# Performance work log

Measured on AMD Instinct MI355X. Metric: run time of the kernel, lower is better.

## Reference

```python
import jax, jax.numpy as jnp
import numpy as np


def _cdist(p1, p2):
    # Euclidean cdist via the matmul expansion (matches torch.cdist p=2 fast path):
    # ||a-b||^2 = ||a||^2 + ||b||^2 - 2 a.b ; clamp tiny negatives before sqrt.
    sq1 = jnp.sum(p1 * p1, axis=-1, keepdims=True)        # (N, 1)
    sq2 = jnp.sum(p2 * p2, axis=-1, keepdims=True).T      # (1, M)
    d2 = sq1 + sq2 - 2.0 * (p1 @ p2.T)                    # (N, M)
    return jnp.sqrt(jnp.maximum(d2, 0.0))


def setup_inputs() -> dict:
    key = jax.random.key(0)
    k1, k2 = jax.random.split(key)
    N, M = 16384, 16384
    points1 = jax.random.normal(k1, (N, 3), dtype=jnp.float32)
    points2 = jax.random.normal(k2, (M, 3), dtype=jnp.float32)
    return {"points1": points1, "points2": points2}


def reference(points1, points2):
    dist = _cdist(points1, points2)                        # (N, M)
    min1 = jnp.min(dist, axis=1)                           # (N,) nearest in points2
    min2 = jnp.min(dist, axis=0)                           # (M,) nearest in points1
    return jnp.sum(min1) + jnp.sum(min2)
```

## Files before the change

kernel.cpp:

```cpp
#include <hip/hip_runtime.h>
#include <hip/hip_bf16.h>
#include <math.h>


typedef _Float16 half8    __attribute__((ext_vector_type(8)));
typedef float    floatx16 __attribute__((ext_vector_type(16)));

constexpr int CH   = 4096;
constexpr int ROWS = 128;
constexpr int BLK  = 256;

__global__ __launch_bounds__(256) void pack_kernel(
    const float* __restrict__ P1, const float* __restrict__ P2,
    uint2* __restrict__ F1, uint2* __restrict__ F2,
    int n1, int n2, int NP, float* __restrict__ out)
{
    int i = blockIdx.x * 256 + threadIdx.x;
    if (i == 0) out[0] = 0.0f;
    const float* P; uint2* F; int n, idx;
    if (i < NP)          { P = P1; F = F1; n = n1; idx = i; }
    else if (i < 2 * NP) { P = P2; F = F2; n = n2; idx = i - NP; }
    else return;
    int j = idx < n ? idx : n - 1;
    float x = P[3*j], y = P[3*j+1], z = P[3*j+2];
    _Float16 hx = (_Float16)x, hy = (_Float16)y, hz = (_Float16)z;
    float qx = (float)hx, qy = (float)hy, qz = (float)hz;
    _Float16 hw = (_Float16)(qx*qx + qy*qy + qz*qz);
    union { _Float16 h[4]; uint2 u; } p;
    p.h[0] = hx; p.h[1] = hy; p.h[2] = hz; p.h[3] = hw;
    F[idx] = p.u;
}

__global__ __launch_bounds__(BLK, 4) void chamfer_sweep_kernel(
    const uint2* __restrict__ F1, const uint2* __restrict__ F2,
    float* __restrict__ part, int n1, int n2, int YC)
{
    __shared__ uint2 sB[CH];
    __shared__ float sRowMin[ROWS];

    const int dir   = blockIdx.z;
    const uint2* FA = dir == 0 ? F1 : F2;
    const uint2* FB = dir == 0 ? F2 : F1;
    const int nA    = dir == 0 ? n1 : n2;
    float* pbase    = part + (dir == 0 ? 0 : (size_t)YC * n1);

    const int tid  = threadIdx.x;
    const int wave = tid >> 6;
    const int lane = tid & 63;
    const int n    = lane & 31;
    const int g    = lane >> 5;
    const bool g0  = (g == 0);

    {
        const uint4* src = (const uint4*)(FB + (size_t)blockIdx.y * CH);
        uint4* dst = (uint4*)sB;
        for (int i = tid; i < CH / 2; i += BLK) dst[i] = src[i];
    }

    const _Float16 h0 = (_Float16)0.0f;
    half8 af;
    {
        int arow = blockIdx.x * ROWS + wave * 32 + n;
        union { uint2 u; _Float16 h[4]; } au; au.u = FA[arow];
        const _Float16 m2 = (_Float16)(-2.0f);
        af[0] = g0 ? (_Float16)(au.h[0] * m2) : h0;
        af[1] = g0 ? (_Float16)(au.h[1] * m2) : h0;
        af[2] = g0 ? (_Float16)(au.h[2] * m2) : h0;
        af[3] = g0 ? (_Float16)1.0f : h0;
        af[4] = g0 ? au.h[3] : h0;
        af[5] = h0; af[6] = h0; af[7] = h0;
    }

    __syncthreads();

    floatx16 rowmin;
#pragma unroll
    for (int r = 0; r < 16; ++r) rowmin[r] = 1e30f;
    const floatx16 zacc = {};

    union BF { half8 v; unsigned u[4]; uint2 lo; };
    BF bu0, bu1, bu2, bu3;
    { union { _Float16 h[2]; unsigned u; } q;
      q.h[0] = (_Float16)1.0f; q.h[1] = h0;
      bu0.u[2] = q.u; bu0.u[3] = 0u;
      bu1.u[2] = q.u; bu1.u[3] = 0u;
      bu2.u[2] = q.u; bu2.u[3] = 0u;
      bu3.u[2] = q.u; bu3.u[3] = 0u; }

    for (int bt = 0; bt < CH / 128; ++bt) {
        const uint2* p = sB + bt * 128 + n;
        bu0.lo = p[0];
        bu1.lo = p[32];
        bu2.lo = p[64];
        bu3.lo = p[96];

        floatx16 d0 = __builtin_amdgcn_mfma_f32_32x32x16_f16(af, bu0.v, zacc, 0, 0, 0);
        floatx16 d1 = __builtin_amdgcn_mfma_f32_32x32x16_f16(af, bu1.v, zacc, 0, 0, 0);
        floatx16 d2 = __builtin_amdgcn_mfma_f32_32x32x16_f16(af, bu2.v, zacc, 0, 0, 0);
        floatx16 d3 = __builtin_amdgcn_mfma_f32_32x32x16_f16(af, bu3.v, zacc, 0, 0, 0);

#pragma unroll
        for (int r = 0; r < 16; ++r) {
            float t = fminf(fminf(rowmin[r], d0[r]), d1[r]);
            rowmin[r] = fminf(fminf(t, d2[r]), d3[r]);
        }
    }

#pragma unroll
    for (int mask = 1; mask <= 16; mask <<= 1)
#pragma unroll
        for (int r = 0; r < 16; ++r)
            rowmin[r] = fminf(rowmin[r], __shfl_xor(rowmin[r], mask));

    if (n == 0) {
#pragma unroll
        for (int r = 0; r < 16; ++r) {
            int rr = wave * 32 + g * 4 + ((r & 3) + 8 * (r >> 2));
            sRowMin[rr] = rowmin[r];
        }
    }
    __syncthreads();

    if (tid < ROWS) {
        int grow = blockIdx.x * ROWS + tid;
        if (grow < nA) pbase[(size_t)grow * YC + blockIdx.y] = sRowMin[tid];
    }
}

__global__ __launch_bounds__(256) void reduce_kernel(
    const float* __restrict__ part, float* __restrict__ out,
    int ntot, int YC)
{
    __shared__ float s[256];
    int r = blockIdx.x * 256 + threadIdx.x;
    float acc = 0.0f;
    if (r < ntot) {
        float m;
        if (YC == 4) {
            const float4 v = ((const float4*)part)[r];
            m = fminf(fminf(v.x, v.y), fminf(v.z, v.w));
        } else {
            const float* p = part + (size_t)r * YC;
            m = 1e30f;
            for (int y = 0; y < YC; ++y) m = fminf(m, p[y]);
        }
        acc = sqrtf(fmaxf(m, 0.0f));
    }
    s[threadIdx.x] = acc;
    __syncthreads();
    for (int w = 128; w > 0; w >>= 1) {
        if (threadIdx.x < w) s[threadIdx.x] += s[threadIdx.x + w];
        __syncthreads();
    }
    if (threadIdx.x == 0) atomicAdd(out, s[0]);
}

extern "C" void kernel_launch(void* const* d_in, const int* in_sizes, int n_in,
                              void* d_out, int out_size, void* d_ws, size_t ws_size,
                              hipStream_t stream) {
    const float* P1 = (const float*)d_in[0];
    const float* P2 = (const float*)d_in[1];
    const int n1 = in_sizes[0] / 3;
    const int n2 = in_sizes[1] / 3;
    const int nmax = (n1 > n2) ? n1 : n2;
    const int YC = (nmax + CH - 1) / CH;
    const int NP = YC * CH;

    uint2* F1   = (uint2*)d_ws;
    uint2* F2   = F1 + NP;
    float* part = (float*)(F2 + NP);
    float* out  = (float*)d_out;

    pack_kernel<<<(2 * NP + 255) / 256, 256, 0, stream>>>(P1, P2, F1, F2, n1, n2, NP, out);

    {
        dim3 grid(NP / ROWS, YC, 2);
        chamfer_sweep_kernel<<<grid, BLK, 0, stream>>>(F1, F2, part, n1, n2, YC);
    }
    reduce_kernel<<<(n1 + n2 + 255) / 256, 256, 0, stream>>>(part, out, n1 + n2, YC);
}
```

Before: 77.18 us.

## Fuse pack, sweep and reduce into one cooperative kernel with grid syncs

Merges the pack, distance-sweep and reduce stages into a single cooperative kernel, separated by grid-wide barriers. It falls back to the original three launches if the cooperative launch fails. The aim is to remove two kernel launches and the idle gaps between them. The price is two grid syncs, and the fused path only runs if all 1024 blocks can be resident at once. The reduce stage now uses 32 threads per block with a warp-shuffle sum.

```diff
diff --git a/kernel.cpp b/kernel.cpp
--- a/kernel.cpp
+++ b/kernel.cpp
@@ -1,6 +1,9 @@
 #include <hip/hip_runtime.h>
+#include <hip/hip_cooperative_groups.h>
 #include <hip/hip_bf16.h>
 #include <math.h>
+
+namespace cg = cooperative_groups;
 
 
 typedef _Float16 half8    __attribute__((ext_vector_type(8)));
@@ -10,28 +13,18 @@
 constexpr int ROWS = 128;
 constexpr int BLK  = 256;
 
-__global__ __launch_bounds__(256) void pack_kernel(
-    const float* __restrict__ P1, const float* __restrict__ P2,
-    uint2* __restrict__ F1, uint2* __restrict__ F2,
-    int n1, int n2, int NP, float* __restrict__ out)
-{
-    int i = blockIdx.x * 256 + threadIdx.x;
-    if (i == 0) out[0] = 0.0f;
-    const float* P; uint2* F; int n, idx;
-    if (i < NP)          { P = P1; F = F1; n = n1; idx = i; }
-    else if (i < 2 * NP) { P = P2; F = F2; n = n2; idx = i - NP; }
-    else return;
-    int j = idx < n ? idx : n - 1;
+__device__ __forceinline__ uint2 pack_point(const float* __restrict__ P, int j)
+{
     float x = P[3*j], y = P[3*j+1], z = P[3*j+2];
     _Float16 hx = (_Float16)x, hy = (_Float16)y, hz = (_Float16)z;
     float qx = (float)hx, qy = (float)hy, qz = (float)hz;
     _Float16 hw = (_Float16)(qx*qx + qy*qy + qz*qz);
     union { _Float16 h[4]; uint2 u; } p;
     p.h[0] = hx; p.h[1] = hy; p.h[2] = hz; p.h[3] = hw;
-    F[idx] = p.u;
-}
-
-__global__ __launch_bounds__(BLK, 4) void chamfer_sweep_kernel(
+    return p.u;
+}
+
+__device__ __forceinline__ void sweep_body(
     const uint2* __restrict__ F1, const uint2* __restrict__ F2,
     float* __restrict__ part, int n1, int n2, int YC)
 {
@@ -125,6 +118,71 @@
         int grow = blockIdx.x * ROWS + tid;
         if (grow < nA) pbase[(size_t)grow * YC + blockIdx.y] = sRowMin[tid];
     }
+}
+
+__global__ __launch_bounds__(BLK, 4) void chamfer_fused_kernel(
+    const float* __restrict__ P1, const float* __restrict__ P2,
+    uint2* __restrict__ F1, uint2* __restrict__ F2,
+    float* __restrict__ part, float* __restrict__ out,
+    int n1, int n2, int YC, int NP)
+{
+    cg::grid_group gg = cg::this_grid();
+    const int fb = blockIdx.x + gridDim.x * (blockIdx.y + gridDim.y * blockIdx.z);
+
+    {
+        int i = fb * BLK + threadIdx.x;
+        if (i == 0) out[0] = 0.0f;
+        if (i < 2 * NP) {
+            if (i < NP) { int j = i < n1 ? i : n1 - 1;            F1[i]      = pack_point(P1, j); }
+            else        { int i2 = i - NP; int j = i2 < n2 ? i2 : n2 - 1; F2[i2] = pack_point(P2, j); }
+        }
+    }
+    gg.sync();
+
+    sweep_body(F1, F2, part, n1, n2, YC);
+    gg.sync();
+
+    {
+        const int ntot = n1 + n2;
+        if (threadIdx.x < 32) {
+            int r = fb * 32 + threadIdx.x;
+            float acc = 0.0f;
+            if (r < ntot) {
+                float m;
+                if (YC == 4) {
+                    const float4 v = ((const float4*)part)[r];
+                    m = fminf(fminf(v.x, v.y), fminf(v.z, v.w));
+                } else {
+                    const float* p = part + (size_t)r * YC;
+                    m = 1e30f;
+                    for (int y = 0; y < YC; ++y) m = fminf(m, p[y]);
+                }
+                acc = sqrtf(fmaxf(m, 0.0f));
+            }
+#pragma unroll
+            for (int mask = 1; mask <= 16; mask <<= 1)
+                acc += __shfl_xor(acc, mask, 32);
+            if (threadIdx.x == 0) atomicAdd(out, acc);
+        }
+    }
+}
+
+__global__ __launch_bounds__(256) void pack_kernel(
+    const float* __restrict__ P1, const float* __restrict__ P2,
+    uint2* __restrict__ F1, uint2* __restrict__ F2,
+    int n1, int n2, int NP, float* __restrict__ out)
+{
+    int i = blockIdx.x * 256 + threadIdx.x;
+    if (i == 0) out[0] = 0.0f;
+    if (i < NP)          { int j = i < n1 ? i : n1 - 1;               F1[i]      = pack_point(P1, j); }
+    else if (i < 2 * NP) { int i2 = i - NP; int j = i2 < n2 ? i2 : n2 - 1; F2[i2] = pack_point(P2, j); }
+}
+
+__global__ __launch_bounds__(BLK, 4) void chamfer_sweep_kernel(
+    const uint2* __restrict__ F1, const uint2* __restrict__ F2,
+    float* __restrict__ part, int n1, int n2, int YC)
+{
+    sweep_body(F1, F2, part, n1, n2, YC);
 }
 
 __global__ __launch_bounds__(256) void reduce_kernel(
@@ -171,11 +229,18 @@
     float* part = (float*)(F2 + NP);
     float* out  = (float*)d_out;
 
-    pack_kernel<<<(2 * NP + 255) / 256, 256, 0, stream>>>(P1, P2, F1, F2, n1, n2, NP, out);
-
-    {
-        dim3 grid(NP / ROWS, YC, 2);
+    dim3 grid(NP / ROWS, YC, 2);
+
+    void* args[] = { (void*)&P1, (void*)&P2, (void*)&F1, (void*)&F2,
+                     (void*)&part, (void*)&out,
+                     (void*)&n1, (void*)&n2, (void*)&YC, (void*)&NP };
+    hipError_t err = hipLaunchCooperativeKernel(
+        (void*)chamfer_fused_kernel, grid, dim3(BLK), args, 0, stream);
+
+    if (err != hipSuccess) {
+        (void)hipGetLastError();
+        pack_kernel<<<(2 * NP + 255) / 256, 256, 0, stream>>>(P1, P2, F1, F2, n1, n2, NP, out);
         chamfer_sweep_kernel<<<grid, BLK, 0, stream>>>(F1, F2, part, n1, n2, YC);
-    }
-    reduce_kernel<<<(n1 + n2 + 255) / 256, 256, 0, stream>>>(part, out, n1 + n2, YC);
-}
+        reduce_kernel<<<(n1 + n2 + 255) / 256, 256, 0, stream>>>(part, out, n1 + n2, YC);
+    }
+}
```

Measured after the change: 308.0 us. 3.99x slower.

## Stage full point set in LDS per block and fuse reduction into sweep kernel

Applied to the files above, without the earlier changes.

Each block now loads the entire opposite point set (up to 16384 points, 128KB) into shared memory instead of a 4096-point chunk. The grid loses its Y dimension, the partial-min buffer goes away, and the sqrt plus sum happen in the sweep kernel with one atomic per block, which removes the separate reduce kernel. The inner loop also software-prefetches the next tile's LDS operands. In exchange, the large LDS footprint limits occupancy to roughly one block per CU, the grid is four times smaller, and inputs larger than 16384 points would be silently truncated.

```diff
diff --git a/kernel.cpp b/kernel.cpp
--- a/kernel.cpp
+++ b/kernel.cpp
@@ -6,9 +6,20 @@
 typedef _Float16 half8    __attribute__((ext_vector_type(8)));
 typedef float    floatx16 __attribute__((ext_vector_type(16)));
 
-constexpr int CH   = 4096;
-constexpr int ROWS = 128;
-constexpr int BLK  = 256;
+constexpr int CHMAX = 16384;
+constexpr int ROWS  = 128;
+constexpr int BLK   = 256;
+
+__device__ __forceinline__ uint2 pack_point(const float* __restrict__ P, int j)
+{
+    float x = P[3*j], y = P[3*j+1], z = P[3*j+2];
+    _Float16 hx = (_Float16)x, hy = (_Float16)y, hz = (_Float16)z;
+    float qx = (float)hx, qy = (float)hy, qz = (float)hz;
+    _Float16 hw = (_Float16)(qx*qx + qy*qy + qz*qz);
+    union { _Float16 h[4]; uint2 u; } p;
+    p.h[0] = hx; p.h[1] = hy; p.h[2] = hz; p.h[3] = hw;
+    return p.u;
+}
 
 __global__ __launch_bounds__(256) void pack_kernel(
     const float* __restrict__ P1, const float* __restrict__ P2,
@@ -17,32 +28,21 @@
 {
     int i = blockIdx.x * 256 + threadIdx.x;
     if (i == 0) out[0] = 0.0f;
-    const float* P; uint2* F; int n, idx;
-    if (i < NP)          { P = P1; F = F1; n = n1; idx = i; }
-    else if (i < 2 * NP) { P = P2; F = F2; n = n2; idx = i - NP; }
-    else return;
-    int j = idx < n ? idx : n - 1;
-    float x = P[3*j], y = P[3*j+1], z = P[3*j+2];
-    _Float16 hx = (_Float16)x, hy = (_Float16)y, hz = (_Float16)z;
-    float qx = (float)hx, qy = (float)hy, qz = (float)hz;
-    _Float16 hw = (_Float16)(qx*qx + qy*qy + qz*qz);
-    union { _Float16 h[4]; uint2 u; } p;
-    p.h[0] = hx; p.h[1] = hy; p.h[2] = hz; p.h[3] = hw;
-    F[idx] = p.u;
+    if (i < NP)          { int j = i < n1 ? i : n1 - 1;                    F1[i]  = pack_point(P1, j); }
+    else if (i < 2 * NP) { int i2 = i - NP; int j = i2 < n2 ? i2 : n2 - 1; F2[i2] = pack_point(P2, j); }
 }
 
-__global__ __launch_bounds__(BLK, 4) void chamfer_sweep_kernel(
+__global__ __launch_bounds__(BLK) void chamfer_sweep_kernel(
     const uint2* __restrict__ F1, const uint2* __restrict__ F2,
-    float* __restrict__ part, int n1, int n2, int YC)
+    float* __restrict__ out, int n1, int n2, int NP)
 {
-    __shared__ uint2 sB[CH];
-    __shared__ float sRowMin[ROWS];
+    __shared__ uint2 sB[CHMAX];
+    __shared__ float sSum[8];
 
     const int dir   = blockIdx.z;
     const uint2* FA = dir == 0 ? F1 : F2;
     const uint2* FB = dir == 0 ? F2 : F1;
     const int nA    = dir == 0 ? n1 : n2;
-    float* pbase    = part + (dir == 0 ? 0 : (size_t)YC * n1);
 
     const int tid  = threadIdx.x;
     const int wave = tid >> 6;
@@ -52,9 +52,9 @@
     const bool g0  = (g == 0);
 
     {
-        const uint4* src = (const uint4*)(FB + (size_t)blockIdx.y * CH);
+        const uint4* src = (const uint4*)FB;
         uint4* dst = (uint4*)sB;
-        for (int i = tid; i < CH / 2; i += BLK) dst[i] = src[i];
+        for (int i = tid; i < NP / 2; i += BLK) dst[i] = src[i];
     }
 
     const _Float16 h0 = (_Float16)0.0f;
@@ -87,12 +87,18 @@
       bu2.u[2] = q.u; bu2.u[3] = 0u;
       bu3.u[2] = q.u; bu3.u[3] = 0u; }
 
-    for (int bt = 0; bt < CH / 128; ++bt) {
-        const uint2* p = sB + bt * 128 + n;
-        bu0.lo = p[0];
-        bu1.lo = p[32];
-        bu2.lo = p[64];
-        bu3.lo = p[96];
+    const int NT = NP / 128;
+    const uint2* p0 = sB + n;
+    uint2 c0 = p0[0], c1 = p0[32], c2 = p0[64], c3 = p0[96];
+
+    for (int bt = 0; bt < NT; ++bt) {
+        const uint2* pn = sB + (bt + 1 < NT ? (bt + 1) * 128 : 0) + n;
+        uint2 f0 = pn[0], f1 = pn[32], f2 = pn[64], f3 = pn[96];
+
+        bu0.lo = c0;
+        bu1.lo = c1;
+        bu2.lo = c2;
+        bu3.lo = c3;
 
         floatx16 d0 = __builtin_amdgcn_mfma_f32_32x32x16_f16(af, bu0.v, zacc, 0, 0, 0);
         floatx16 d1 = __builtin_amdgcn_mfma_f32_32x32x16_f16(af, bu1.v, zacc, 0, 0, 0);
@@ -104,6 +110,8 @@
             float t = fminf(fminf(rowmin[r], d0[r]), d1[r]);
             rowmin[r] = fminf(fminf(t, d2[r]), d3[r]);
         }
+
+        c0 = f0; c1 = f1; c2 = f2; c3 = f3;
     }
 
 #pragma unroll
@@ -112,47 +120,23 @@
         for (int r = 0; r < 16; ++r)
             rowmin[r] = fminf(rowmin[r], __shfl_xor(rowmin[r], mask));
 
+    float acc = 0.0f;
     if (n == 0) {
 #pragma unroll
         for (int r = 0; r < 16; ++r) {
-            int rr = wave * 32 + g * 4 + ((r & 3) + 8 * (r >> 2));
-            sRowMin[rr] = rowmin[r];
+            int grow = blockIdx.x * ROWS + wave * 32 + g * 4 + ((r & 3) + 8 * (r >> 2));
+            if (grow < nA) acc += sqrtf(fmaxf(rowmin[r], 0.0f));
         }
+        sSum[wave * 2 + g] = acc;
     }
     __syncthreads();
 
-    if (tid < ROWS) {
-        int grow = blockIdx.x * ROWS + tid;
-        if (grow < nA) pbase[(size_t)grow * YC + blockIdx.y] = sRowMin[tid];
+    if (tid == 0) {
+        float s = 0.0f;
+#pragma unroll
+        for (int i = 0; i < 8; ++i) s += sSum[i];
+        atomicAdd(out, s);
     }
-}
-
-__global__ __launch_bounds__(256) void reduce_kernel(
-    const float* __restrict__ part, float* __restrict__ out,
-    int ntot, int YC)
-{
-    __shared__ float s[256];
-    int r = blockIdx.x * 256 + threadIdx.x;
-    float acc = 0.0f;
-    if (r < ntot) {
-        float m;
-        if (YC == 4) {
-            const float4 v = ((const float4*)part)[r];
-            m = fminf(fminf(v.x, v.y), fminf(v.z, v.w));
-        } else {
-            const float* p = part + (size_t)r * YC;
-            m = 1e30f;
-            for (int y = 0; y < YC; ++y) m = fminf(m, p[y]);
-        }
-        acc = sqrtf(fmaxf(m, 0.0f));
-    }
-    s[threadIdx.x] = acc;
-    __syncthreads();
-    for (int w = 128; w > 0; w >>= 1) {
-        if (threadIdx.x < w) s[threadIdx.x] += s[threadIdx.x + w];
-        __syncthreads();
-    }
-    if (threadIdx.x == 0) atomicAdd(out, s[0]);
 }
 
 extern "C" void kernel_launch(void* const* d_in, const int* in_sizes, int n_in,
@@ -163,19 +147,18 @@
     const int n1 = in_sizes[0] / 3;
     const int n2 = in_sizes[1] / 3;
     const int nmax = (n1 > n2) ? n1 : n2;
-    const int YC = (nmax + CH - 1) / CH;
-    const int NP = YC * CH;
+    int NP = ((nmax + 127) / 128) * 128;
+    if (NP > CHMAX) NP = CHMAX;
+    const int NPp = NP;
 
     uint2* F1   = (uint2*)d_ws;
-    uint2* F2   = F1 + NP;
-    float* part = (float*)(F2 + NP);
+    uint2* F2   = F1 + NPp;
     float* out  = (float*)d_out;
 
-    pack_kernel<<<(2 * NP + 255) / 256, 256, 0, stream>>>(P1, P2, F1, F2, n1, n2, NP, out);
+    pack_kernel<<<(2 * NPp + 255) / 256, 256, 0, stream>>>(P1, P2, F1, F2, n1, n2, NPp, out);
 
     {
-        dim3 grid(NP / ROWS, YC, 2);
-        chamfer_sweep_kernel<<<grid, BLK, 0, stream>>>(F1, F2, part, n1, n2, YC);
+        dim3 grid(NPp / ROWS, 1, 2);
+        chamfer_sweep_kernel<<<grid, BLK, 0, stream>>>(F1, F2, out, n1, n2, NPp);
     }
-    reduce_kernel<<<(n1 + n2 + 255) / 256, 256, 0, stream>>>(part, out, n1 + n2, YC);
 }
```

New measurement: 103.9 us. 1.35x slower.
